# Kernel optimization log

Hardware: AMD Instinct MI355X
Metric: run time of the kernel (lower is better)

The kernel has to match this reference:

```python
import jax, jax.numpy as jnp
import numpy as np

B, T, N, C = 4, 2048, 4, 1024   # batch, seq, expansion_rate, hidden_dim
A = 8                            # max_lora_adapters
SINKHORN_ITERS = 20
EPS = 1e-05


def _logit(x):
    x = jnp.clip(x, 1e-06, 1.0 - 1e-06)
    return jnp.log(x) - jnp.log(1.0 - x)


def setup_inputs() -> dict:
    key = jax.random.key(0)
    ks = jax.random.split(key, 12)
    nC = N * C
    x = jax.random.normal(ks[0], (B, T, N, C), dtype=jnp.float32)
    adapter_indices = jax.random.randint(ks[1], (B,), 0, A)
    # Learned parameters (perturbed from the identity init so gradients are non-trivial)
    input_norm_weight = 1.0 + 0.02 * jax.random.normal(ks[2], (A, nC), dtype=jnp.float32)
    phi_pre = 0.02 * jax.random.normal(ks[3], (A, nC, N), dtype=jnp.float32)
    phi_post = 0.02 * jax.random.normal(ks[4], (A, nC, N), dtype=jnp.float32)
    phi_res = 0.02 * jax.random.normal(ks[5], (A, nC, N * N), dtype=jnp.float32)
    b_pre = _logit(jnp.float32(1.0 / N)) + 0.1 * jax.random.normal(ks[6], (A, N), dtype=jnp.float32)
    b_post = 0.1 * jax.random.normal(ks[7], (A, N), dtype=jnp.float32)
    b_res = 10.0 * jnp.eye(N, dtype=jnp.float32) + jax.random.normal(ks[8], (A, N, N), dtype=jnp.float32)
    alpha_pre = 1.0 + 0.1 * jax.random.normal(ks[9], (A,), dtype=jnp.float32)
    alpha_post = 1.0 + 0.1 * jax.random.normal(ks[10], (A,), dtype=jnp.float32)
    alpha_res = 1.0 + 0.1 * jax.random.normal(ks[11], (A,), dtype=jnp.float32)
    return {
        "x": x,
        "input_norm_weight": input_norm_weight,
        "phi_pre": phi_pre, "phi_post": phi_post, "phi_res": phi_res,
        "b_pre": b_pre, "b_post": b_post, "b_res": b_res,
        "alpha_pre": alpha_pre, "alpha_post": alpha_post, "alpha_res": alpha_res,
        "adapter_indices": adapter_indices,
    }


def _sinkhorn_knopp(M, iters):
    M = jnp.exp(M)
    def step(_, mat):
        mat = mat / mat.sum(axis=-1, keepdims=True)
        mat = mat / mat.sum(axis=-2, keepdims=True)
        return mat
    return jax.lax.fori_loop(0, iters, step, M)


def reference(x, input_norm_weight, phi_pre, phi_post, phi_res,
              b_pre, b_post, b_res, alpha_pre, alpha_post, alpha_res,
              adapter_indices):
    Bb, Tt, n, Cc = x.shape
    idx = adapter_indices.astype(jnp.int32)
    x_flat = x.reshape(Bb, Tt, n * Cc)
    # adapter-indexed RMSNorm
    w = input_norm_weight[idx]                                  # [B, nC]
    rms = jnp.sqrt(jnp.mean(x_flat ** 2, axis=-1, keepdims=True) + EPS)
    x_norm = w[:, None, :] * x_flat / rms                       # [B, T, nC]
    # pre: input-dependent aggregation weights H_pre
    pre_logits = jnp.einsum('btd,bdn->btn', x_norm, phi_pre[idx])
    H_pre = jax.nn.sigmoid(alpha_pre[idx][:, None, None] * pre_logits + b_pre[idx][:, None, :])
    x_agg = (H_pre[..., None] * x).sum(axis=-2)                 # [B, T, C]
    output = x_agg                                              # identity block between pre and post
    # post: distribution weights H_post and doubly-stochastic mixing M
    post_logits = jnp.einsum('btd,bdn->btn', x_norm, phi_post[idx])
    H_post = 2.0 * jax.nn.sigmoid(alpha_post[idx][:, None, None] * post_logits + b_post[idx][:, None, :])
    res_logits = jnp.einsum('btd,bdm->btm', x_norm, phi_res[idx]).reshape(Bb, Tt, n, n)
    tilde_H_res = alpha_res[idx][:, None, None, None] * res_logits + b_res[idx][:, None, :, :]
    M = _sinkhorn_knopp(tilde_H_res, SINKHORN_ITERS)            # [B, T, n, n]
    y_dist = H_post[..., None] * output[..., None, :]           # [B, T, n, C]
    x_mixed = jnp.einsum('btij,btjc->btic', M, x)               # [B, T, n, C]
    return x_mixed + y_dist
```

## Files before the change

kernel.cpp:

```cpp
#include <hip/hip_runtime.h>


#define BT 8192
#define NC 4096
#define NC4 1024
#define NT 32
#define TD 128

__global__ __launch_bounds__(256) void lora_w_kernel(
    const float* __restrict__ x,
    const float* __restrict__ inw,
    const float* __restrict__ phi_pre,
    const float* __restrict__ phi_post,
    const float* __restrict__ phi_res,
    const float* __restrict__ b_pre,
    const float* __restrict__ b_post,
    const float* __restrict__ b_res,
    const float* __restrict__ alpha_pre,
    const float* __restrict__ alpha_post,
    const float* __restrict__ alpha_res,
    const int*   __restrict__ adapter_indices,
    float* __restrict__ wsf)
{
    const int tid = threadIdx.x;
    const int g   = tid & 3;
    const int wvid= tid >> 6;
    const int ln  = tid & 63;
    const int dl  = tid & 127;
    const int half= tid >> 7;
    const int blk = blockIdx.x;
    const int b   = blk >> 9;
    const int idx = adapter_indices[b];

    const float4* __restrict__ pp4 = (const float4*)(phi_pre  + (size_t)idx * (NC * 4));
    const float4* __restrict__ po4 = (const float4*)(phi_post + (size_t)idx * (NC * 4));
    const float4* __restrict__ pr4 = (const float4*)(phi_res  + (size_t)idx * (NC * 16));
    const float*  __restrict__ inwp = inw + (size_t)idx * NC + dl;
    const float*  __restrict__ xb   = x + (size_t)(blk * 4) * NC + dl;

    __shared__ float4 tileL[2][768];
    __shared__ float red[4][4][14];

    const float4* sg[3];
    int sstr[3];
    #pragma unroll
    for (int i = 0; i < 3; ++i) {
        const int c = wvid * 3 + i;
        const float4* bp; int off, str;
        if (c < 4) {
            bp  = (c < 2) ? pp4 : po4;
            off = ((c & 1) << 6) + ln;
            str = TD;
        } else {
            const int k = c - 4;
            bp  = pr4;
            off = ((((k & 1) << 6) + ln) << 2) + (k >> 1);
            str = TD * 4;
        }
        sg[i] = bp + off;
        sstr[i] = str;
    }

    #define STAGE_TILE(MT, BF)                                                   \
    {                                                                            \
        _Pragma("unroll")                                                        \
        for (int i = 0; i < 3; ++i) {                                            \
            __builtin_amdgcn_global_load_lds(                                    \
                (const __attribute__((address_space(1))) void*)(sg[i] + (size_t)(MT) * sstr[i]), \
                (__attribute__((address_space(3))) void*)&tileL[BF][((wvid * 3 + i) << 6) + ln], \
                16, 0, 0);                                                       \
        }                                                                        \
    }

    STAGE_TILE(0, 0);

    float acc[12][4];
    float ss[4];
    #pragma unroll
    for (int j = 0; j < 12; ++j) {
        acc[j][0] = 0.0f; acc[j][1] = 0.0f; acc[j][2] = 0.0f; acc[j][3] = 0.0f;
    }
    ss[0] = ss[1] = ss[2] = ss[3] = 0.0f;

    float xn[4], wn;
    #pragma unroll
    for (int j = 0; j < 4; ++j) xn[j] = xb[j * NC];
    wn = inwp[0];

    const int ba = half * 384 + dl;

    #pragma unroll 1
    for (int m = 0; m < NT; ++m) {
        const int bf = m & 1;
        __syncthreads();
        if (m < NT - 1) STAGE_TILE(m + 1, bf ^ 1);

        const float wv = wn;
        float s[4];
        #pragma unroll
        for (int j = 0; j < 4; ++j) {
            const float xv = xn[j];
            s[j] = xv * wv;
            ss[j] = fmaf(xv, xv, ss[j]);
        }
        if (m < NT - 1) {
            #pragma unroll
            for (int j = 0; j < 4; ++j) xn[j] = xb[j * NC + (m + 1) * TD];
            wn = inwp[(m + 1) * TD];
        }

        const float4 a = tileL[bf][ba];
        const float4 p = tileL[bf][ba + 128];
        const float4 r = tileL[bf][ba + 256];
        #pragma unroll
        for (int j = 0; j < 4; ++j) {
            acc[0][j]  = fmaf(s[j], a.x, acc[0][j]);
            acc[1][j]  = fmaf(s[j], a.y, acc[1][j]);
            acc[2][j]  = fmaf(s[j], a.z, acc[2][j]);
            acc[3][j]  = fmaf(s[j], a.w, acc[3][j]);
            acc[4][j]  = fmaf(s[j], p.x, acc[4][j]);
            acc[5][j]  = fmaf(s[j], p.y, acc[5][j]);
            acc[6][j]  = fmaf(s[j], p.z, acc[6][j]);
            acc[7][j]  = fmaf(s[j], p.w, acc[7][j]);
            acc[8][j]  = fmaf(s[j], r.x, acc[8][j]);
            acc[9][j]  = fmaf(s[j], r.y, acc[9][j]);
            acc[10][j] = fmaf(s[j], r.z, acc[10][j]);
            acc[11][j] = fmaf(s[j], r.w, acc[11][j]);
        }
    }

    float t12[13];
    #define RED4(V0, V1, V2, V3, DST)                                   \
    {                                                                   \
        const float u0 = (V0) + __shfl_xor((V0), 1);                    \
        const float u1 = (V1) + __shfl_xor((V1), 1);                    \
        const float u2 = (V2) + __shfl_xor((V2), 1);                    \
        const float u3 = (V3) + __shfl_xor((V3), 1);                    \
        const float r0 = (ln & 1) ? u1 : u0;                            \
        const float r1 = (ln & 1) ? u3 : u2;                            \
        const float w0 = r0 + __shfl_xor(r0, 2);                        \
        const float w1 = r1 + __shfl_xor(r1, 2);                        \
        float tv = (ln & 2) ? w1 : w0;                                  \
        tv += __shfl_xor(tv, 4);  tv += __shfl_xor(tv, 8);              \
        tv += __shfl_xor(tv, 16); tv += __shfl_xor(tv, 32);             \
        (DST) = tv;                                                     \
    }
    #pragma unroll
    for (int j = 0; j < 12; ++j)
        RED4(acc[j][0], acc[j][1], acc[j][2], acc[j][3], t12[j]);
    RED4(ss[0], ss[1], ss[2], ss[3], t12[12]);
    #undef RED4

    if (ln < 4) {
        #pragma unroll
        for (int j = 0; j < 13; ++j) red[wvid][ln][j] = t12[j];
    }
    __syncthreads();
    float tot[25];
    #pragma unroll
    for (int j = 0; j < 12; ++j) {
        tot[j]      = red[0][g][j] + red[1][g][j];
        tot[12 + j] = red[2][g][j] + red[3][g][j];
    }
    tot[24] = red[0][g][12] + red[1][g][12];

    const float inv_rms = rsqrtf(tot[24] * (1.0f / 4096.0f) + 1e-5f);
    const float apre  = alpha_pre[idx];
    const float apost = alpha_post[idx];
    const float ares  = alpha_res[idx];

    float Hpre[4], Hpost[4];
    #pragma unroll
    for (int n = 0; n < 4; ++n) {
        const float zp = fmaf(apre,  tot[n]     * inv_rms, b_pre[idx * 4 + n]);
        Hpre[n]  = 1.0f / (1.0f + __expf(-zp));
        const float zq = fmaf(apost, tot[4 + n] * inv_rms, b_post[idx * 4 + n]);
        Hpost[n] = 2.0f / (1.0f + __expf(-zq));
    }

    const int s16 = ln >> 2;
    const int sj = s16 & 3;
    const int si = s16 >> 2;
    float Mv = __expf(fmaf(ares, tot[8 + si * 4 + sj] * inv_rms,
                           b_res[idx * 16 + si * 4 + sj]));
    #pragma unroll
    for (int it = 0; it < 20; ++it) {
        float rs = Mv + __shfl_xor(Mv, 4);
        rs += __shfl_xor(rs, 8);
        Mv *= __builtin_amdgcn_rcpf(rs);
        float cs = Mv + __shfl_xor(Mv, 16);
        cs += __shfl_xor(cs, 32);
        Mv *= __builtin_amdgcn_rcpf(cs);
    }

    if (wvid == 0) {
        const float hpo = (si == 0) ? Hpost[0] : (si == 1) ? Hpost[1]
                        : (si == 2) ? Hpost[2] : Hpost[3];
        const float hpr = (sj == 0) ? Hpre[0]  : (sj == 1) ? Hpre[1]
                        : (sj == 2) ? Hpre[2]  : Hpre[3];
        wsf[(size_t)blk * 64 + g * 16 + si * 4 + sj] = fmaf(hpo, hpr, Mv);
    }
    #undef STAGE_TILE
}

__global__ __launch_bounds__(256) void lora_mix_kernel(
    const float* __restrict__ x,
    const float* __restrict__ wsf,
    float* __restrict__ out)
{
    const int tok = blockIdx.x;
    const int c4  = threadIdx.x;

    const float4* __restrict__ x4p = (const float4*)x   + (size_t)tok * NC4;
    float4* __restrict__       out4 = (float4*)out      + (size_t)tok * NC4;
    const float4* __restrict__ w4   = (const float4*)wsf + (size_t)tok * 4;

    const float4 W0 = w4[0];
    const float4 W1 = w4[1];
    const float4 W2 = w4[2];
    const float4 W3 = w4[3];

    const float4 x0 = x4p[0 * 256 + c4];
    const float4 x1 = x4p[1 * 256 + c4];
    const float4 x2 = x4p[2 * 256 + c4];
    const float4 x3 = x4p[3 * 256 + c4];

    #define MIXROW(WR, DSTIDX)                                                    \
    {                                                                             \
        float4 o;                                                                 \
        o.x = fmaf(WR.x, x0.x, fmaf(WR.y, x1.x, fmaf(WR.z, x2.x, WR.w * x3.x)));  \
        o.y = fmaf(WR.x, x0.y, fmaf(WR.y, x1.y, fmaf(WR.z, x2.y, WR.w * x3.y)));  \
        o.z = fmaf(WR.x, x0.z, fmaf(WR.y, x1.z, fmaf(WR.z, x2.z, WR.w * x3.z)));  \
        o.w = fmaf(WR.x, x0.w, fmaf(WR.y, x1.w, fmaf(WR.z, x2.w, WR.w * x3.w)));  \
        out4[(DSTIDX) * 256 + c4] = o;                                            \
    }
    MIXROW(W0, 0);
    MIXROW(W1, 1);
    MIXROW(W2, 2);
    MIXROW(W3, 3);
    #undef MIXROW
}

extern "C" void kernel_launch(void* const* d_in, const int* in_sizes, int n_in,
                              void* d_out, int out_size, void* d_ws, size_t ws_size,
                              hipStream_t stream) {
    const float* x         = (const float*)d_in[0];
    const float* inw       = (const float*)d_in[1];
    const float* phi_pre   = (const float*)d_in[2];
    const float* phi_post  = (const float*)d_in[3];
    const float* phi_res   = (const float*)d_in[4];
    const float* b_pre     = (const float*)d_in[5];
    const float* b_post    = (const float*)d_in[6];
    const float* b_res     = (const float*)d_in[7];
    const float* alpha_pre = (const float*)d_in[8];
    const float* alpha_post= (const float*)d_in[9];
    const float* alpha_res = (const float*)d_in[10];
    const int*   adapter   = (const int*)d_in[11];
    float* out = (float*)d_out;
    float* wsf = (float*)d_ws;

    dim3 block(256);
    lora_w_kernel<<<dim3(BT / 4), block, 0, stream>>>(
        x, inw, phi_pre, phi_post, phi_res,
        b_pre, b_post, b_res,
        alpha_pre, alpha_post, alpha_res,
        adapter, wsf);
    lora_mix_kernel<<<dim3(BT), block, 0, stream>>>(x, wsf, out);
}
```

Before: 318.5 us.

## Split projection reduction over feature chunks and move Sinkhorn into mix kernel

The first kernel now splits the 4096-wide feature reduction into 4 chunks across 4x more blocks, each writing partial sums (pre, post, res logits and sum of squares) to workspace. The mix kernel then sums the chunk partials, computes the RMS, sigmoids and Sinkhorn iterations for each token in one wave, and shares the mixing weights through LDS before the output pass. This raises parallelism in the reduction kernel, whose 2048 blocks each ran a long serial loop. In exchange the mix kernel gains a serial Sinkhorn prologue plus a block sync, and workspace traffic grows.

Result: no change. 323.6 us (+1.6%).

```diff
diff --git a/kernel.cpp b/kernel.cpp
--- a/kernel.cpp
+++ b/kernel.cpp
@@ -4,39 +4,34 @@
 #define BT 8192
 #define NC 4096
 #define NC4 1024
-#define NT 32
+#define NTC 8
 #define TD 128
 
-__global__ __launch_bounds__(256) void lora_w_kernel(
+__global__ __launch_bounds__(256) void lora_partial_kernel(
     const float* __restrict__ x,
     const float* __restrict__ inw,
     const float* __restrict__ phi_pre,
     const float* __restrict__ phi_post,
     const float* __restrict__ phi_res,
-    const float* __restrict__ b_pre,
-    const float* __restrict__ b_post,
-    const float* __restrict__ b_res,
-    const float* __restrict__ alpha_pre,
-    const float* __restrict__ alpha_post,
-    const float* __restrict__ alpha_res,
     const int*   __restrict__ adapter_indices,
     float* __restrict__ wsf)
 {
     const int tid = threadIdx.x;
-    const int g   = tid & 3;
     const int wvid= tid >> 6;
     const int ln  = tid & 63;
     const int dl  = tid & 127;
     const int half= tid >> 7;
     const int blk = blockIdx.x;
-    const int b   = blk >> 9;
+    const int chunk = blk >> 11;
+    const int tg    = blk & 2047;
+    const int b   = tg >> 9;
     const int idx = adapter_indices[b];
 
-    const float4* __restrict__ pp4 = (const float4*)(phi_pre  + (size_t)idx * (NC * 4));
-    const float4* __restrict__ po4 = (const float4*)(phi_post + (size_t)idx * (NC * 4));
-    const float4* __restrict__ pr4 = (const float4*)(phi_res  + (size_t)idx * (NC * 16));
-    const float*  __restrict__ inwp = inw + (size_t)idx * NC + dl;
-    const float*  __restrict__ xb   = x + (size_t)(blk * 4) * NC + dl;
+    const float4* __restrict__ pp4 = (const float4*)(phi_pre  + (size_t)idx * (NC * 4))  + (size_t)chunk * 1024;
+    const float4* __restrict__ po4 = (const float4*)(phi_post + (size_t)idx * (NC * 4))  + (size_t)chunk * 1024;
+    const float4* __restrict__ pr4 = (const float4*)(phi_res  + (size_t)idx * (NC * 16)) + (size_t)chunk * 4096;
+    const float*  __restrict__ inwp = inw + (size_t)idx * NC + chunk * 1024 + dl;
+    const float*  __restrict__ xb   = x + (size_t)(tg * 4) * NC + chunk * 1024 + dl;
 
     __shared__ float4 tileL[2][768];
     __shared__ float red[4][4][14];
@@ -90,10 +85,10 @@
     const int ba = half * 384 + dl;
 
     #pragma unroll 1
-    for (int m = 0; m < NT; ++m) {
+    for (int m = 0; m < NTC; ++m) {
         const int bf = m & 1;
         __syncthreads();
-        if (m < NT - 1) STAGE_TILE(m + 1, bf ^ 1);
+        if (m < NTC - 1) STAGE_TILE(m + 1, bf ^ 1);
 
         const float wv = wn;
         float s[4];
@@ -103,7 +98,7 @@
             s[j] = xv * wv;
             ss[j] = fmaf(xv, xv, ss[j]);
         }
-        if (m < NT - 1) {
+        if (m < NTC - 1) {
             #pragma unroll
             for (int j = 0; j < 4; ++j) xn[j] = xb[j * NC + (m + 1) * TD];
             wn = inwp[(m + 1) * TD];
@@ -156,49 +151,12 @@
         for (int j = 0; j < 13; ++j) red[wvid][ln][j] = t12[j];
     }
     __syncthreads();
-    float tot[25];
-    #pragma unroll
-    for (int j = 0; j < 12; ++j) {
-        tot[j]      = red[0][g][j] + red[1][g][j];
-        tot[12 + j] = red[2][g][j] + red[3][g][j];
-    }
-    tot[24] = red[0][g][12] + red[1][g][12];
-
-    const float inv_rms = rsqrtf(tot[24] * (1.0f / 4096.0f) + 1e-5f);
-    const float apre  = alpha_pre[idx];
-    const float apost = alpha_post[idx];
-    const float ares  = alpha_res[idx];
-
-    float Hpre[4], Hpost[4];
-    #pragma unroll
-    for (int n = 0; n < 4; ++n) {
-        const float zp = fmaf(apre,  tot[n]     * inv_rms, b_pre[idx * 4 + n]);
-        Hpre[n]  = 1.0f / (1.0f + __expf(-zp));
-        const float zq = fmaf(apost, tot[4 + n] * inv_rms, b_post[idx * 4 + n]);
-        Hpost[n] = 2.0f / (1.0f + __expf(-zq));
-    }
-
-    const int s16 = ln >> 2;
-    const int sj = s16 & 3;
-    const int si = s16 >> 2;
-    float Mv = __expf(fmaf(ares, tot[8 + si * 4 + sj] * inv_rms,
-                           b_res[idx * 16 + si * 4 + sj]));
-    #pragma unroll
-    for (int it = 0; it < 20; ++it) {
-        float rs = Mv + __shfl_xor(Mv, 4);
-        rs += __shfl_xor(rs, 8);
-        Mv *= __builtin_amdgcn_rcpf(rs);
-        float cs = Mv + __shfl_xor(Mv, 16);
-        cs += __shfl_xor(cs, 32);
-        Mv *= __builtin_amdgcn_rcpf(cs);
-    }
-
-    if (wvid == 0) {
-        const float hpo = (si == 0) ? Hpost[0] : (si == 1) ? Hpost[1]
-                        : (si == 2) ? Hpost[2] : Hpost[3];
-        const float hpr = (sj == 0) ? Hpre[0]  : (sj == 1) ? Hpre[1]
-                        : (sj == 2) ? Hpre[2]  : Hpre[3];
-        wsf[(size_t)blk * 64 + g * 16 + si * 4 + sj] = fmaf(hpo, hpr, Mv);
+    if (tid < 100) {
+        const int gg = tid / 25;
+        const int j  = tid % 25;
+        const float v = (j < 13) ? (red[0][gg][j] + red[1][gg][j])
+                                 : (red[2][gg][j - 13] + red[3][gg][j - 13]);
+        wsf[((size_t)(tg * 4 + gg) * 4 + chunk) * 26 + j] = v;
     }
     #undef STAGE_TILE
 }
@@ -206,24 +164,65 @@
 __global__ __launch_bounds__(256) void lora_mix_kernel(
     const float* __restrict__ x,
     const float* __restrict__ wsf,
+    const float* __restrict__ b_pre,
+    const float* __restrict__ b_post,
+    const float* __restrict__ b_res,
+    const float* __restrict__ alpha_pre,
+    const float* __restrict__ alpha_post,
+    const float* __restrict__ alpha_res,
+    const int*   __restrict__ adapter_indices,
     float* __restrict__ out)
 {
     const int tok = blockIdx.x;
-    const int c4  = threadIdx.x;
-
-    const float4* __restrict__ x4p = (const float4*)x   + (size_t)tok * NC4;
-    float4* __restrict__       out4 = (float4*)out      + (size_t)tok * NC4;
-    const float4* __restrict__ w4   = (const float4*)wsf + (size_t)tok * 4;
-
-    const float4 W0 = w4[0];
-    const float4 W1 = w4[1];
-    const float4 W2 = w4[2];
-    const float4 W3 = w4[3];
-
-    const float4 x0 = x4p[0 * 256 + c4];
-    const float4 x1 = x4p[1 * 256 + c4];
-    const float4 x2 = x4p[2 * 256 + c4];
-    const float4 x3 = x4p[3 * 256 + c4];
+    const int tid = threadIdx.x;
+
+    const float4* __restrict__ x4p = (const float4*)x + (size_t)tok * NC4;
+    float4* __restrict__       out4 = (float4*)out    + (size_t)tok * NC4;
+
+    __shared__ float4 Wl4[4];
+
+    const float4 x0 = x4p[0 * 256 + tid];
+    const float4 x1 = x4p[1 * 256 + tid];
+    const float4 x2 = x4p[2 * 256 + tid];
+    const float4 x3 = x4p[3 * 256 + tid];
+
+    if (tid < 64) {
+        const int rj = tid >> 2;
+        const int sj = rj & 3;
+        const int si = rj >> 2;
+        const int idx = adapter_indices[tok >> 11];
+        const float* __restrict__ base = wsf + (size_t)tok * 104;
+        const int rslot = (rj < 4) ? (8 + rj) : (9 + rj);
+        float pre_s = 0.0f, post_s = 0.0f, res_s = 0.0f, ss_s = 0.0f;
+        #pragma unroll
+        for (int c = 0; c < 4; ++c) {
+            pre_s  += base[c * 26 + sj];
+            post_s += base[c * 26 + 4 + si];
+            res_s  += base[c * 26 + rslot];
+            ss_s   += base[c * 26 + 12];
+        }
+        const float inv_rms = rsqrtf(ss_s * (1.0f / 4096.0f) + 1e-5f);
+        const float Hpre_j  = 1.0f / (1.0f + __expf(-fmaf(alpha_pre[idx],  pre_s  * inv_rms, b_pre[idx * 4 + sj])));
+        const float Hpost_i = 2.0f / (1.0f + __expf(-fmaf(alpha_post[idx], post_s * inv_rms, b_post[idx * 4 + si])));
+        float Mv = __expf(fmaf(alpha_res[idx], res_s * inv_rms, b_res[idx * 16 + rj]));
+        #pragma unroll
+        for (int it = 0; it < 20; ++it) {
+            float rs = Mv + __shfl_xor(Mv, 4);
+            rs += __shfl_xor(rs, 8);
+            Mv *= __builtin_amdgcn_rcpf(rs);
+            float cs = Mv + __shfl_xor(Mv, 16);
+            cs += __shfl_xor(cs, 32);
+            Mv *= __builtin_amdgcn_rcpf(cs);
+        }
+        if ((tid & 3) == 0)
+            ((float*)Wl4)[rj] = fmaf(Hpost_i, Hpre_j, Mv);
+    }
+    __syncthreads();
+
+    const float4 W0 = Wl4[0];
+    const float4 W1 = Wl4[1];
+    const float4 W2 = Wl4[2];
+    const float4 W3 = Wl4[3];
 
     #define MIXROW(WR, DSTIDX)                                                    \
     {                                                                             \
@@ -232,7 +231,7 @@
         o.y = fmaf(WR.x, x0.y, fmaf(WR.y, x1.y, fmaf(WR.z, x2.y, WR.w * x3.y)));  \
         o.z = fmaf(WR.x, x0.z, fmaf(WR.y, x1.z, fmaf(WR.z, x2.z, WR.w * x3.z)));  \
         o.w = fmaf(WR.x, x0.w, fmaf(WR.y, x1.w, fmaf(WR.z, x2.w, WR.w * x3.w)));  \
-        out4[(DSTIDX) * 256 + c4] = o;                                            \
+        out4[(DSTIDX) * 256 + tid] = o;                                           \
     }
     MIXROW(W0, 0);
     MIXROW(W1, 1);
@@ -260,10 +259,9 @@
     float* wsf = (float*)d_ws;
 
     dim3 block(256);
-    lora_w_kernel<<<dim3(BT / 4), block, 0, stream>>>(
-        x, inw, phi_pre, phi_post, phi_res,
-        b_pre, b_post, b_res,
-        alpha_pre, alpha_post, alpha_res,
-        adapter, wsf);
-    lora_mix_kernel<<<dim3(BT), block, 0, stream>>>(x, wsf, out);
+    lora_partial_kernel<<<dim3(BT * 4 / 4), block, 0, stream>>>(
+        x, inw, phi_pre, phi_post, phi_res, adapter, wsf);
+    lora_mix_kernel<<<dim3(BT), block, 0, stream>>>(
+        x, wsf, b_pre, b_post, b_res,
+        alpha_pre, alpha_post, alpha_res, adapter, out);
 }
```
